# Kernel tuning notes

Hardware: AMD Instinct MI355X
Metric: run time of the kernel (lower is better)

Reference implementation:

```python
import jax, jax.numpy as jnp
import numpy as np

N = 4096      # num nodes == lr feature dim
H = 8         # heads
HR = 256
C = 2 * HR    # heads * head_dim = 512
D = C // H    # head_dim = 64
EPS = 1e-5


def setup_inputs() -> dict:
    key = jax.random.key(0)
    ks = jax.random.split(key, 10)
    s_in = 1.0 / np.sqrt(N)
    inp = {
        "x": jax.random.normal(ks[0], (N, N), jnp.float32),
        "Wq": jax.random.normal(ks[1], (N, C), jnp.float32) * s_in,
        "bq": jax.random.normal(ks[2], (C,), jnp.float32) * 0.02,
        "Wk": jax.random.normal(ks[3], (N, C), jnp.float32) * s_in,
        "bk": jax.random.normal(ks[4], (C,), jnp.float32) * 0.02,
        "Wv": jax.random.normal(ks[5], (N, C), jnp.float32) * s_in,
        "bv": jax.random.normal(ks[6], (C,), jnp.float32) * 0.02,
        "we": jax.random.normal(ks[7], (C,), jnp.float32),
        "Wskip": jax.random.normal(ks[8], (N, C), jnp.float32) * s_in,
        "bskip": jax.random.normal(ks[9], (C,), jnp.float32) * 0.02,
        "gn_w": jnp.ones((C,), jnp.float32),
        "gn_b": jnp.zeros((C,), jnp.float32),
        "gn_ms": jnp.ones((C,), jnp.float32),
    }
    return inp


def reference(x, Wq, bq, Wk, bk, Wv, bv, we, Wskip, bskip, gn_w, gn_b, gn_ms):
    # TransformerConv on a fully-connected graph; edge (src=j -> tgt=i) attr = x[j, i].
    q = (x @ Wq + bq).reshape(N, H, D)
    k = (x @ Wk + bk).reshape(N, H, D)
    v = (x @ Wv + bv).reshape(N, H, D)
    we_h = we.reshape(H, D)                      # lin_edge weight (no bias)

    xa = x.T                                     # xa[i, j] = edge attr of j -> i
    qk = jnp.einsum('ihd,jhd->ijh', q, k)        # [N, N, H]
    qe = jnp.einsum('ihd,hd->ih', q, we_h)       # [N, H]
    scores = (qk + xa[:, :, None] * qe[:, None, :]) / jnp.sqrt(jnp.float32(D))
    alpha = jax.nn.softmax(scores, axis=1)       # softmax over sources j

    out = jnp.einsum('ijh,jhd->ihd', alpha, v)   # sum_j alpha * value_j
    s = jnp.einsum('ijh,ij->ih', alpha, xa)      # sum_j alpha * edge_attr
    out = out + s[:, :, None] * we_h[None]       # edge embedding added to value too
    out = out.reshape(N, C) + (x @ Wskip + bskip)  # root/skip connection

    # GraphNorm (single graph): per-channel stats over nodes
    mean = out.mean(axis=0)
    centered = out - gn_ms * mean
    var = jnp.mean(centered * centered, axis=0)
    out = gn_w * centered / jnp.sqrt(var + EPS) + gn_b

    # per-node L2 normalization
    out = out / jnp.sqrt(jnp.sum(out * out, axis=1, keepdims=True))
    return out
```

## Files before the change

### kernel.cpp

```cpp
#include <hip/hip_runtime.h>


typedef short s8v __attribute__((ext_vector_type(8)));
typedef unsigned short u16x8 __attribute__((ext_vector_type(8)));
typedef unsigned short u16x4 __attribute__((ext_vector_type(4)));
typedef float f4 __attribute__((ext_vector_type(4)));
typedef unsigned short u16;

__device__ __forceinline__ u16 f2bf(float f) {
    union { float f; unsigned u; } v; v.f = f;
    unsigned r = v.u + 0x7fffu + ((v.u >> 16) & 1u);
    return (u16)(r >> 16);
}
__device__ __forceinline__ u16 f2bf_hu(float f) {
    union { float f; unsigned u; } v; v.f = f;
    return (u16)((v.u + 0x8000u) >> 16);
}
__device__ __forceinline__ float bf2f(u16 h) {
    union { unsigned u; float f; } v; v.u = ((unsigned)h) << 16;
    return v.f;
}

#define GLD16(g, l) __builtin_amdgcn_global_load_lds( \
    (const __attribute__((address_space(1))) void*)(g), \
    (__attribute__((address_space(3))) void*)(l), 16, 0, 0)

__global__ __launch_bounds__(256) void k_convx(const float* __restrict__ x,
                                               u16* __restrict__ xb,
                                               float* __restrict__ stats) {
    if (blockIdx.x == 0) {
        int t = threadIdx.x;
        stats[t] = 0.f; stats[256 + t] = 0.f; stats[512 + t] = 0.f; stats[768 + t] = 0.f;
    }
    size_t i = ((size_t)blockIdx.x * 256 + threadIdx.x) * 8;
    float4 a = *(const float4*)(x + i);
    float4 b = *(const float4*)(x + i + 4);
    u16x8 o;
    o[0]=f2bf(a.x); o[1]=f2bf(a.y); o[2]=f2bf(a.z); o[3]=f2bf(a.w);
    o[4]=f2bf(b.x); o[5]=f2bf(b.y); o[6]=f2bf(b.z); o[7]=f2bf(b.w);
    *(u16x8*)(xb + i) = o;
}

__global__ __launch_bounds__(256) void k_transw(const float* __restrict__ Wq,
                                                const float* __restrict__ Wk,
                                                const float* __restrict__ Wv,
                                                const float* __restrict__ Ws,
                                                u16* __restrict__ wb) {
    __shared__ float tile[64][65];
    int k0 = blockIdx.x * 64;
    int n0 = blockIdx.y * 64;
    const float* W = (n0 < 512) ? Wq : (n0 < 1024) ? Wk : (n0 < 1536) ? Wv : Ws;
    int col0 = n0 & 511;
    int t = threadIdx.x;
#pragma unroll
    for (int q = 0; q < 4; q++) {
        int idx = t + 256 * q;
        int row = idx >> 4, c4 = (idx & 15) * 4;
        float4 v = *(const float4*)&W[(size_t)(k0 + row) * 512 + col0 + c4];
        tile[row][c4 + 0] = v.x; tile[row][c4 + 1] = v.y;
        tile[row][c4 + 2] = v.z; tile[row][c4 + 3] = v.w;
    }
    __syncthreads();
#pragma unroll
    for (int q = 0; q < 2; q++) {
        int idx = t + 256 * q;
        int row = idx >> 3, c8 = (idx & 7) * 8;
        u16x8 o;
#pragma unroll
        for (int j = 0; j < 8; j++) o[j] = f2bf(tile[c8 + j][row]);
        *(u16x8*)&wb[(size_t)(n0 + row) * 4096 + k0 + c8] = o;
    }
}

__global__ __launch_bounds__(512) void k_gemm(const u16* __restrict__ xb,
                                              const u16* __restrict__ wb,
                                              const float* __restrict__ bq,
                                              const float* __restrict__ bk,
                                              const float* __restrict__ bv,
                                              const float* __restrict__ bs,
                                              u16* __restrict__ qkvs,
                                              u16* __restrict__ vt) {
    __shared__ __align__(16) u16 A_lds[128 * 64];
    __shared__ __align__(16) u16 B_lds[128 * 64];
    int tid = threadIdx.x;
    int w = tid >> 6, lane = tid & 63;
    int wr = w >> 1, wc = w & 1;
    int L = lane & 15, q = lane >> 4;
    int m0 = blockIdx.y * 128, n0 = blockIdx.x * 128;

    const f4 fz = {0.f, 0.f, 0.f, 0.f};
    f4 acc[2][4];
#pragma unroll
    for (int r = 0; r < 2; r++)
#pragma unroll
        for (int t = 0; t < 4; t++) acc[r][t] = fz;

    int r8 = lane >> 3;
    int csw = ((lane & 7) ^ r8) * 8;
    const u16* gS;
    u16* lds_s;
    int rb0;
    if (w < 4) { gS = xb + (size_t)(m0 + r8) * 4096 + csw; lds_s = A_lds; rb0 = 32 * w; }
    else       { gS = wb + (size_t)(n0 + r8) * 4096 + csw; lds_s = B_lds; rb0 = 32 * (w - 4); }

    for (int kt = 0; kt < 64; ++kt) {
        int k0 = kt * 64;
#pragma unroll
        for (int g = 0; g < 4; g++) {
            int rb = rb0 + 8 * g;
            GLD16(gS + (size_t)rb * 4096 + k0, &lds_s[rb * 64]);
        }
        __syncthreads();
        s8v a[2][2], b[4][2];
#pragma unroll
        for (int r = 0; r < 2; r++) {
            int row = wr * 32 + 16 * r + L;
            int r7 = row & 7;
            a[r][0] = *(const s8v*)&A_lds[row * 64 + ((q ^ r7) * 8)];
            a[r][1] = *(const s8v*)&A_lds[row * 64 + (((4 + q) ^ r7) * 8)];
        }
#pragma unroll
        for (int t = 0; t < 4; t++) {
            int row = wc * 64 + 16 * t + L;
            int r7 = row & 7;
            b[t][0] = *(const s8v*)&B_lds[row * 64 + ((q ^ r7) * 8)];
            b[t][1] = *(const s8v*)&B_lds[row * 64 + (((4 + q) ^ r7) * 8)];
        }
#pragma unroll
        for (int r = 0; r < 2; r++)
#pragma unroll
            for (int t = 0; t < 4; t++) {
                acc[r][t] = __builtin_amdgcn_mfma_f32_16x16x32_bf16(a[r][0], b[t][0], acc[r][t], 0, 0, 0);
                acc[r][t] = __builtin_amdgcn_mfma_f32_16x16x32_bf16(a[r][1], b[t][1], acc[r][t], 0, 0, 0);
            }
        __syncthreads();
    }

#pragma unroll
    for (int t = 0; t < 4; t++) {
        int n = n0 + wc * 64 + 16 * t + L;
        int seg = n >> 9, o = n & 511;
        const float* bp = (seg == 0) ? bq : (seg == 1) ? bk : (seg == 2) ? bv : bs;
        float bias = bp[o];
        float scale = (seg == 0) ? 0.1803368801f : 1.f;
#pragma unroll
        for (int r = 0; r < 2; r++) {
            int mbase = m0 + wr * 32 + 16 * r + 4 * q;
            u16x4 hv;
#pragma unroll
            for (int q2 = 0; q2 < 4; q2++) {
                u16 hb = f2bf((acc[r][t][q2] + bias) * scale);
                hv[q2] = hb;
                qkvs[(size_t)(mbase + q2) * 2048 + n] = hb;
            }
            if (seg == 2)
                *(u16x4*)&vt[(size_t)(n - 1024) * 4096 + mbase] = hv;
        }
    }
}

__global__ __launch_bounds__(256, 4) void k_attn(const u16* __restrict__ qkvs,
                                                 const u16* __restrict__ xb,
                                                 const u16* __restrict__ vt,
                                                 const float* __restrict__ we,
                                                 float* __restrict__ o_part,
                                                 float* __restrict__ lsa_part) {
    __shared__ __align__(16) u16 K_lds[64 * 64];
    __shared__ __align__(16) u16 V_lds[64 * 64];
    __shared__ __align__(16) u16 P_lds[64 * 72];
    __shared__ __align__(16) u16 X_lds[64 * 72];
    __shared__ float qe8[64];

    int tid = threadIdx.x;
    int w = tid >> 6, lane = tid & 63;
    int L = lane & 15, q = lane >> 4;
    int i0 = blockIdx.x * 64;
    int h = blockIdx.y, hc = h * 64;
    int sp = blockIdx.z;

    int r8 = lane >> 3;
    int csw = ((lane & 7) ^ r8) * 8;

    {
        const u16* g0 = qkvs + (size_t)i0 * 2048 + hc;
#pragma unroll
        for (int ih = 0; ih < 2; ih++) {
            int rb = 16 * w + 8 * ih;
            GLD16(g0 + (size_t)(rb + r8) * 2048 + csw, &K_lds[rb * 64]);
        }
    }
    __syncthreads();

    s8v qf[2];
#pragma unroll
    for (int c = 0; c < 2; c++) {
        int row = 16 * w + L;
        qf[c] = *(const s8v*)&K_lds[row * 64 + (((4 * c + q) ^ (row & 7)) * 8)];
    }
    if (tid < 64) {
        float s = 0.f;
        int r7 = tid & 7;
#pragma unroll
        for (int d = 0; d < 64; d++)
            s += bf2f(K_lds[tid * 64 + ((d >> 3) ^ r7) * 8 + (d & 7)]) * we[hc + d];
        qe8[tid] = s;
    }
    __syncthreads();

    float qe_r[4];
#pragma unroll
    for (int r = 0; r < 4; r++) qe_r[r] = qe8[16 * w + 4 * q + r];

    const f4 fz = {0.f, 0.f, 0.f, 0.f};
    f4 o_acc[4];
    float l_p[4], sa_p[4];
#pragma unroll
    for (int r = 0; r < 4; r++) { l_p[r] = 0.f; sa_p[r] = 0.f; }
#pragma unroll
    for (int t = 0; t < 4; t++) o_acc[t] = fz;

    for (int jt64 = 0; jt64 < 32; ++jt64) {
        int j0 = sp * 2048 + jt64 * 64;
        {
            const u16* g0 = qkvs + (size_t)j0 * 2048 + 512 + hc;
#pragma unroll
            for (int ih = 0; ih < 2; ih++) {
                int rb = 16 * w + 8 * ih;
                GLD16(g0 + (size_t)(rb + r8) * 2048 + csw, &K_lds[rb * 64]);
            }
        }
        {
            const u16* g0 = vt + (size_t)hc * 4096 + j0;
#pragma unroll
            for (int ih = 0; ih < 2; ih++) {
                int rb = 16 * w + 8 * ih;
                GLD16(g0 + (size_t)(rb + r8) * 4096 + csw, &V_lds[rb * 64]);
            }
        }
#pragma unroll
        for (int qq = 0; qq < 2; qq++) {
            int idx = tid + 256 * qq;
            int row = idx >> 3, c8 = (idx & 7) * 8;
            *(s8v*)&X_lds[row * 72 + c8] =
                *(const s8v*)&xb[(size_t)(j0 + row) * 4096 + i0 + c8];
        }
        __syncthreads();

#pragma unroll
        for (int jt = 0; jt < 4; jt++) {
            int n = L + 16 * jt;
            int n7 = n & 7;
            s8v b0 = *(const s8v*)&K_lds[n * 64 + ((q ^ n7) * 8)];
            s8v b1 = *(const s8v*)&K_lds[n * 64 + (((4 + q) ^ n7) * 8)];
            f4 acc = fz;
            acc = __builtin_amdgcn_mfma_f32_16x16x32_bf16(qf[0], b0, acc, 0, 0, 0);
            acc = __builtin_amdgcn_mfma_f32_16x16x32_bf16(qf[1], b1, acc, 0, 0, 0);
            u16x4 xv4 = *(const u16x4*)&X_lds[n * 72 + 16 * w + 4 * q];
#pragma unroll
            for (int r = 0; r < 4; r++) {
                float xx = bf2f(xv4[r]);
                float s = fminf(acc[r] + xx * qe_r[r], 115.f);
                float p = __builtin_amdgcn_exp2f(s);
                l_p[r] += p;
                sa_p[r] += p * xx;
                P_lds[(16 * w + 4 * q + r) * 72 + n] = f2bf_hu(p);
            }
        }

        {
            int row = 16 * w + L;
            s8v a0 = *(const s8v*)&P_lds[row * 72 + q * 8];
            s8v a1 = *(const s8v*)&P_lds[row * 72 + 32 + q * 8];
#pragma unroll
            for (int t = 0; t < 4; t++) {
                int n = L + 16 * t;
                int n7 = n & 7;
                s8v b0 = *(const s8v*)&V_lds[n * 64 + ((q ^ n7) * 8)];
                s8v b1 = *(const s8v*)&V_lds[n * 64 + (((4 + q) ^ n7) * 8)];
                o_acc[t] = __builtin_amdgcn_mfma_f32_16x16x32_bf16(a0, b0, o_acc[t], 0, 0, 0);
                o_acc[t] = __builtin_amdgcn_mfma_f32_16x16x32_bf16(a1, b1, o_acc[t], 0, 0, 0);
            }
        }
        __syncthreads();
    }

#pragma unroll
    for (int r = 0; r < 4; r++) {
        float l = l_p[r], sa = sa_p[r];
        l += __shfl_xor(l, 1);  sa += __shfl_xor(sa, 1);
        l += __shfl_xor(l, 2);  sa += __shfl_xor(sa, 2);
        l += __shfl_xor(l, 4);  sa += __shfl_xor(sa, 4);
        l += __shfl_xor(l, 8);  sa += __shfl_xor(sa, 8);
        int i = i0 + 16 * w + 4 * q + r;
#pragma unroll
        for (int t = 0; t < 4; t++)
            o_part[((size_t)sp * 4096 + i) * 512 + hc + L + 16 * t] = o_acc[t][r];
        if (L == 0) {
            size_t bi = (((size_t)sp * 4096 + i) * 8 + h) * 2;
            lsa_part[bi] = l;
            lsa_part[bi + 1] = sa;
        }
    }
}

__global__ __launch_bounds__(512) void k_comb(const float* __restrict__ o_part,
                                              const float* __restrict__ lsa,
                                              const u16* __restrict__ qkvs,
                                              const float* __restrict__ we,
                                              float* __restrict__ out_pre,
                                              float* __restrict__ stats) {
    int c = threadIdx.x;
    int r0 = blockIdx.x * 64;
    int h = c >> 6;
    float wec = we[c];
    float s = 0.f, s2 = 0.f;
    for (int ii = 0; ii < 64; ii++) {
        int i = r0 + ii;
        size_t b0 = ((size_t)i * 8 + h) * 2;
        size_t b1 = (((size_t)4096 + i) * 8 + h) * 2;
        float l = lsa[b0] + lsa[b1];
        float sa = lsa[b0 + 1] + lsa[b1 + 1];
        float o = o_part[(size_t)i * 512 + c] + o_part[((size_t)4096 + i) * 512 + c];
        float inv = 1.f / l;
        float v = (o + sa * wec) * inv + bf2f(qkvs[(size_t)i * 2048 + 1536 + c]);
        out_pre[(size_t)i * 512 + c] = v;
        s += v; s2 += v * v;
    }
    atomicAdd(&stats[c], s);
    atomicAdd(&stats[512 + c], s2);
}

__global__ __launch_bounds__(512) void k_final(const float* __restrict__ out_pre,
                                               const float* __restrict__ stats,
                                               const float* __restrict__ gn_w,
                                               const float* __restrict__ gn_b,
                                               const float* __restrict__ gn_ms,
                                               float* __restrict__ out) {
    __shared__ float red[8];
    int c = threadIdx.x;
    int i = blockIdx.x;
    float mean = stats[c] * (1.f / 4096.f);
    float ex2 = stats[512 + c] * (1.f / 4096.f);
    float g = gn_ms[c];
    float var = ex2 - (2.f * g - g * g) * mean * mean;
    float y = gn_w[c] * (out_pre[(size_t)i * 512 + c] - g * mean) * rsqrtf(var + 1e-5f) + gn_b[c];
    float qv = y * y;
    qv += __shfl_xor(qv, 1);  qv += __shfl_xor(qv, 2);  qv += __shfl_xor(qv, 4);
    qv += __shfl_xor(qv, 8);  qv += __shfl_xor(qv, 16); qv += __shfl_xor(qv, 32);
    if ((c & 63) == 0) red[c >> 6] = qv;
    __syncthreads();
    float tot = 0.f;
#pragma unroll
    for (int k = 0; k < 8; k++) tot += red[k];
    out[(size_t)i * 512 + c] = y * rsqrtf(tot);
}

extern "C" void kernel_launch(void* const* d_in, const int* in_sizes, int n_in,
                              void* d_out, int out_size, void* d_ws, size_t ws_size,
                              hipStream_t stream) {
    (void)in_sizes; (void)n_in; (void)out_size; (void)ws_size;
    const float* x    = (const float*)d_in[0];
    const float* Wq   = (const float*)d_in[1];
    const float* bq   = (const float*)d_in[2];
    const float* Wk   = (const float*)d_in[3];
    const float* bk   = (const float*)d_in[4];
    const float* Wv   = (const float*)d_in[5];
    const float* bv   = (const float*)d_in[6];
    const float* we   = (const float*)d_in[7];
    const float* Ws   = (const float*)d_in[8];
    const float* bs   = (const float*)d_in[9];
    const float* gnw  = (const float*)d_in[10];
    const float* gnb  = (const float*)d_in[11];
    const float* gnms = (const float*)d_in[12];
    float* out = (float*)d_out;

    char* ws = (char*)d_ws;
    u16* xb        = (u16*)(ws);
    float* out_pre = (float*)(ws);
    u16* wb        = (u16*)(ws + (size_t)33554432);
    float* o_part  = (float*)(ws + (size_t)33554432);
    u16* qkvs      = (u16*)(ws + (size_t)50331648);
    u16* vt        = (u16*)(ws + (size_t)67108864);
    float* lsa     = (float*)(ws + (size_t)71303168);
    float* stats   = (float*)(ws + (size_t)71303168 + 524288);

    k_convx<<<8192, 256, 0, stream>>>(x, xb, stats);
    k_transw<<<dim3(64, 32), 256, 0, stream>>>(Wq, Wk, Wv, Ws, wb);
    k_gemm<<<dim3(16, 32), 512, 0, stream>>>(xb, wb, bq, bk, bv, bs, qkvs, vt);
    k_attn<<<dim3(64, 8, 2), 256, 0, stream>>>(qkvs, xb, vt, we, o_part, lsa);
    k_comb<<<64, 512, 0, stream>>>(o_part, lsa, qkvs, we, out_pre, stats);
    k_final<<<4096, 512, 0, stream>>>(out_pre, stats, gnw, gnb, gnms, out);
}
```

Measured before the change: 311.6 us.

## Widen attention tiles to 128 rows, split keys three ways, store partials in bf16

The attention kernel now uses 512-thread blocks covering 128 query rows, so each K/V tile loaded into LDS serves twice as many queries. The key range is split into three uneven chunks (22/21/21 tiles) instead of two, giving 768 blocks. Per-split output partials are stored as bf16 to halve that write and read traffic. The combine kernel sums three partials and runs on more, smaller row blocks. The larger block raises LDS and register pressure per workgroup, and bf16 partials lose some precision.

```diff
diff --git a/kernel.cpp b/kernel.cpp
--- a/kernel.cpp
+++ b/kernel.cpp
@@ -159,24 +159,26 @@
     }
 }
 
-__global__ __launch_bounds__(256, 4) void k_attn(const u16* __restrict__ qkvs,
+__global__ __launch_bounds__(512, 6) void k_attn(const u16* __restrict__ qkvs,
                                                  const u16* __restrict__ xb,
                                                  const u16* __restrict__ vt,
                                                  const float* __restrict__ we,
-                                                 float* __restrict__ o_part,
+                                                 u16* __restrict__ o_part,
                                                  float* __restrict__ lsa_part) {
     __shared__ __align__(16) u16 K_lds[64 * 64];
     __shared__ __align__(16) u16 V_lds[64 * 64];
-    __shared__ __align__(16) u16 P_lds[64 * 72];
-    __shared__ __align__(16) u16 X_lds[64 * 72];
-    __shared__ float qe8[64];
+    __shared__ __align__(16) u16 P_lds[128 * 72];
+    __shared__ __align__(16) u16 X_lds[64 * 136];
+    __shared__ float qe_s[128];
 
     int tid = threadIdx.x;
     int w = tid >> 6, lane = tid & 63;
     int L = lane & 15, q = lane >> 4;
-    int i0 = blockIdx.x * 64;
+    int i0 = blockIdx.x * 128;
     int h = blockIdx.y, hc = h * 64;
     int sp = blockIdx.z;
+    int t0 = (sp == 0) ? 0 : (1 + 21 * sp);
+    int tn = sp ? 21 : 22;
 
     int r8 = lane >> 3;
     int csw = ((lane & 7) ^ r8) * 8;
@@ -186,7 +188,7 @@
 #pragma unroll
         for (int ih = 0; ih < 2; ih++) {
             int rb = 16 * w + 8 * ih;
-            GLD16(g0 + (size_t)(rb + r8) * 2048 + csw, &K_lds[rb * 64]);
+            GLD16(g0 + (size_t)(rb + r8) * 2048 + csw, &P_lds[rb * 64]);
         }
     }
     __syncthreads();
@@ -195,21 +197,21 @@
 #pragma unroll
     for (int c = 0; c < 2; c++) {
         int row = 16 * w + L;
-        qf[c] = *(const s8v*)&K_lds[row * 64 + (((4 * c + q) ^ (row & 7)) * 8)];
-    }
-    if (tid < 64) {
+        qf[c] = *(const s8v*)&P_lds[row * 64 + (((4 * c + q) ^ (row & 7)) * 8)];
+    }
+    if (tid < 128) {
         float s = 0.f;
         int r7 = tid & 7;
 #pragma unroll
         for (int d = 0; d < 64; d++)
-            s += bf2f(K_lds[tid * 64 + ((d >> 3) ^ r7) * 8 + (d & 7)]) * we[hc + d];
-        qe8[tid] = s;
+            s += bf2f(P_lds[tid * 64 + ((d >> 3) ^ r7) * 8 + (d & 7)]) * we[hc + d];
+        qe_s[tid] = s;
     }
     __syncthreads();
 
     float qe_r[4];
 #pragma unroll
-    for (int r = 0; r < 4; r++) qe_r[r] = qe8[16 * w + 4 * q + r];
+    for (int r = 0; r < 4; r++) qe_r[r] = qe_s[16 * w + 4 * q + r];
 
     const f4 fz = {0.f, 0.f, 0.f, 0.f};
     f4 o_acc[4];
@@ -219,29 +221,15 @@
 #pragma unroll
     for (int t = 0; t < 4; t++) o_acc[t] = fz;
 
-    for (int jt64 = 0; jt64 < 32; ++jt64) {
-        int j0 = sp * 2048 + jt64 * 64;
-        {
-            const u16* g0 = qkvs + (size_t)j0 * 2048 + 512 + hc;
-#pragma unroll
-            for (int ih = 0; ih < 2; ih++) {
-                int rb = 16 * w + 8 * ih;
-                GLD16(g0 + (size_t)(rb + r8) * 2048 + csw, &K_lds[rb * 64]);
-            }
-        }
-        {
-            const u16* g0 = vt + (size_t)hc * 4096 + j0;
-#pragma unroll
-            for (int ih = 0; ih < 2; ih++) {
-                int rb = 16 * w + 8 * ih;
-                GLD16(g0 + (size_t)(rb + r8) * 4096 + csw, &V_lds[rb * 64]);
-            }
-        }
+    for (int jt64 = 0; jt64 < tn; ++jt64) {
+        int j0 = (t0 + jt64) * 64;
+        GLD16(qkvs + (size_t)(j0 + 8 * w + r8) * 2048 + 512 + hc + csw, &K_lds[8 * w * 64]);
+        GLD16(vt + (size_t)(hc + 8 * w + r8) * 4096 + j0 + csw, &V_lds[8 * w * 64]);
 #pragma unroll
         for (int qq = 0; qq < 2; qq++) {
-            int idx = tid + 256 * qq;
-            int row = idx >> 3, c8 = (idx & 7) * 8;
-            *(s8v*)&X_lds[row * 72 + c8] =
+            int idx = tid + 512 * qq;
+            int row = idx >> 4, c8 = (idx & 15) * 8;
+            *(s8v*)&X_lds[row * 136 + c8] =
                 *(const s8v*)&xb[(size_t)(j0 + row) * 4096 + i0 + c8];
         }
         __syncthreads();
@@ -255,7 +243,7 @@
             f4 acc = fz;
             acc = __builtin_amdgcn_mfma_f32_16x16x32_bf16(qf[0], b0, acc, 0, 0, 0);
             acc = __builtin_amdgcn_mfma_f32_16x16x32_bf16(qf[1], b1, acc, 0, 0, 0);
-            u16x4 xv4 = *(const u16x4*)&X_lds[n * 72 + 16 * w + 4 * q];
+            u16x4 xv4 = *(const u16x4*)&X_lds[n * 136 + 16 * w + 4 * q];
 #pragma unroll
             for (int r = 0; r < 4; r++) {
                 float xx = bf2f(xv4[r]);
@@ -294,7 +282,7 @@
         int i = i0 + 16 * w + 4 * q + r;
 #pragma unroll
         for (int t = 0; t < 4; t++)
-            o_part[((size_t)sp * 4096 + i) * 512 + hc + L + 16 * t] = o_acc[t][r];
+            o_part[((size_t)sp * 4096 + i) * 512 + hc + L + 16 * t] = f2bf(o_acc[t][r]);
         if (L == 0) {
             size_t bi = (((size_t)sp * 4096 + i) * 8 + h) * 2;
             lsa_part[bi] = l;
@@ -303,24 +291,27 @@
     }
 }
 
-__global__ __launch_bounds__(512) void k_comb(const float* __restrict__ o_part,
+__global__ __launch_bounds__(512) void k_comb(const u16* __restrict__ o_part,
                                               const float* __restrict__ lsa,
                                               const u16* __restrict__ qkvs,
                                               const float* __restrict__ we,
                                               float* __restrict__ out_pre,
                                               float* __restrict__ stats) {
     int c = threadIdx.x;
-    int r0 = blockIdx.x * 64;
+    int r0 = blockIdx.x * 16;
     int h = c >> 6;
     float wec = we[c];
     float s = 0.f, s2 = 0.f;
-    for (int ii = 0; ii < 64; ii++) {
+    for (int ii = 0; ii < 16; ii++) {
         int i = r0 + ii;
-        size_t b0 = ((size_t)i * 8 + h) * 2;
-        size_t b1 = (((size_t)4096 + i) * 8 + h) * 2;
-        float l = lsa[b0] + lsa[b1];
-        float sa = lsa[b0 + 1] + lsa[b1 + 1];
-        float o = o_part[(size_t)i * 512 + c] + o_part[((size_t)4096 + i) * 512 + c];
+        float l = 0.f, sa = 0.f, o = 0.f;
+#pragma unroll
+        for (int spp = 0; spp < 3; spp++) {
+            size_t b = (((size_t)spp * 4096 + i) * 8 + h) * 2;
+            l += lsa[b];
+            sa += lsa[b + 1];
+            o += bf2f(o_part[((size_t)spp * 4096 + i) * 512 + c]);
+        }
         float inv = 1.f / l;
         float v = (o + sa * wec) * inv + bf2f(qkvs[(size_t)i * 2048 + 1536 + c]);
         out_pre[(size_t)i * 512 + c] = v;
@@ -378,16 +369,16 @@
     u16* xb        = (u16*)(ws);
     float* out_pre = (float*)(ws);
     u16* wb        = (u16*)(ws + (size_t)33554432);
-    float* o_part  = (float*)(ws + (size_t)33554432);
+    u16* o_part    = (u16*)(ws + (size_t)33554432);
     u16* qkvs      = (u16*)(ws + (size_t)50331648);
     u16* vt        = (u16*)(ws + (size_t)67108864);
     float* lsa     = (float*)(ws + (size_t)71303168);
-    float* stats   = (float*)(ws + (size_t)71303168 + 524288);
+    float* stats   = (float*)(ws + (size_t)71303168 + 786432);
 
     k_convx<<<8192, 256, 0, stream>>>(x, xb, stats);
     k_transw<<<dim3(64, 32), 256, 0, stream>>>(Wq, Wk, Wv, Ws, wb);
     k_gemm<<<dim3(16, 32), 512, 0, stream>>>(xb, wb, bq, bk, bv, bs, qkvs, vt);
-    k_attn<<<dim3(64, 8, 2), 256, 0, stream>>>(qkvs, xb, vt, we, o_part, lsa);
-    k_comb<<<64, 512, 0, stream>>>(o_part, lsa, qkvs, we, out_pre, stats);
+    k_attn<<<dim3(32, 8, 3), 512, 0, stream>>>(qkvs, xb, vt, we, o_part, lsa);
+    k_comb<<<256, 512, 0, stream>>>(o_part, lsa, qkvs, we, out_pre, stats);
     k_final<<<4096, 512, 0, stream>>>(out_pre, stats, gnw, gnb, gnms, out);
 }
```

After: 346.7 us. +11.3%, slower.
